# Kernel tuning notes

Hardware: AMD Instinct MI355X
Metric: run time of the kernel (lower is better)

The kernel has to match this reference:

```python
import jax, jax.numpy as jnp
import numpy as np

N = 100000
E = 1600000
IN_C = 256
OUT_C = 64


def setup_inputs() -> dict:
    key = jax.random.key(0)
    k1, k2, k3, k4, k5 = jax.random.split(key, 5)
    x = jax.random.normal(k1, (N, IN_C), dtype=jnp.float32)
    edge_index = jax.random.randint(k2, (2, E), 0, N, dtype=jnp.int64)
    edge_weight = jax.random.uniform(k3, (E,), dtype=jnp.float32)
    # GCNConv linear weight (Glorot-style scale) and bias
    W = jax.random.normal(k4, (IN_C, OUT_C), dtype=jnp.float32) * (1.0 / np.sqrt(IN_C))
    b = jax.random.normal(k5, (OUT_C,), dtype=jnp.float32) * 0.01
    return {"x": x, "edge_index": edge_index, "edge_weight": edge_weight, "W": W, "b": b}


def reference(x, edge_index, edge_weight, W, b):
    n = x.shape[0]
    row, col = edge_index[0], edge_index[1]  # source -> target (PyG source_to_target flow)
    # add self-loops with weight 1.0 (GCNConv default add_self_loops=True)
    loop = jnp.arange(n, dtype=edge_index.dtype)
    row = jnp.concatenate([row, loop])
    col = jnp.concatenate([col, loop])
    ew = jnp.concatenate([edge_weight, jnp.ones((n,), dtype=x.dtype)])
    # symmetric normalization: deg computed on target nodes
    deg = jax.ops.segment_sum(ew, col, num_segments=n)
    dinv = jnp.where(deg > 0, jax.lax.rsqrt(deg), 0.0)
    norm = dinv[row] * ew * dinv[col]  # [E+N]
    # dense linear transform first (fewer FLOPs than transforming per-edge)
    h = x @ W  # [N, OUT_C]
    # gather messages from source, scale, scatter-add to target
    out = jax.ops.segment_sum(norm[:, None] * h[row], col, num_segments=n)
    out = out + b
    # activation is None -> module returns (val, ()); we return val
    return out
```

## Files before the change

### kernel.cpp

```cpp
#include <hip/hip_runtime.h>
#include <hip/hip_fp16.h>


#define BS 256
#define EPB2 2048
#define BSH 8
#define CAP 4608

typedef unsigned long long u64;
typedef unsigned int u32;
typedef unsigned short u16;
typedef unsigned char u8;

typedef __attribute__((ext_vector_type(8))) short bf16x8;
typedef __attribute__((ext_vector_type(4))) float f32x4;

__device__ inline u16 f2bf(float f) {
    u32 u = __float_as_uint(f);
    return (u16)((u + 0x7fffu + ((u >> 16) & 1u)) >> 16);
}
__device__ inline u32 pack2bf(float a, float b) {
    return (u32)f2bf(a) | ((u32)f2bf(b) << 16);
}

#define GBM2 128
#define XAP 40

__global__ __launch_bounds__(BS) void k_g5(const float* __restrict__ x,
                                           const float* __restrict__ W,
                                           u16* __restrict__ hh, int n, int ngemm,
                                           const int* __restrict__ row,
                                           const int* __restrict__ col,
                                           const float* __restrict__ ew,
                                           u32* __restrict__ cursor,
                                           u64* __restrict__ pack,
                                           int nbuck, int e) {
    __shared__ __align__(16) u8 smem[16384];
    const int tid = threadIdx.x;

    if ((int)blockIdx.x >= ngemm) {
        u16* bkt  = (u16*)smem;
        u16* sidx = (u16*)(smem + 4096);
        u32* cnt  = (u32*)(smem + 8192);
        u32* scn  = (u32*)(smem + 10240);
        u32* lpos = (u32*)(smem + 12288);
        u32* gb   = (u32*)(smem + 14336);
        int blk = blockIdx.x - ngemm;
        int base = blk * EPB2;
        int ej = e - base; if (ej > EPB2) ej = EPB2;

        cnt[tid] = 0; cnt[tid + 256] = 0;
        __syncthreads();
#pragma unroll
        for (int j = 0; j < 8; ++j) {
            int lj = j * BS + tid;
            if (lj < ej) {
                int b = col[base + lj] >> BSH;
                bkt[lj] = (u16)b;
                atomicAdd(&cnt[b], 1u);
            }
        }
        __syncthreads();
        scn[tid] = cnt[tid];
        scn[tid + 256] = cnt[tid + 256];
        __syncthreads();
        for (int off = 1; off < 512; off <<= 1) {
            u32 a0 = (tid >= off) ? scn[tid - off] : 0u;
            u32 a1 = scn[tid + 256 - off];
            __syncthreads();
            scn[tid] += a0;
            scn[tid + 256] += a1;
            __syncthreads();
        }
        for (int t = tid; t < 512; t += 256) {
            u32 c = cnt[t];
            lpos[t] = scn[t] - c;
            if (c) gb[t] = atomicAdd(&cursor[t], c);
        }
        __syncthreads();
#pragma unroll
        for (int j = 0; j < 8; ++j) {
            int lj = j * BS + tid;
            if (lj < ej) {
                u32 p = atomicAdd(&lpos[bkt[lj]], 1u);
                sidx[p] = (u16)lj;
            }
        }
        __syncthreads();
        for (int p = tid; p < ej; p += 256) {
            int lj = sidx[p];
            int b = bkt[lj];
            int i = base + lj;
            __half eh = __float2half(ew[i]);
            u64 en = (u64)(u32)row[i]
                   | ((u64)(u32)(col[i] & 255) << 32)
                   | ((u64)(u16)__half_as_ushort(eh) << 48);
            u32 local = (u32)p - (scn[b] - cnt[b]) + gb[b];
            if (local < CAP) pack[(size_t)b * CAP + local] = en;
        }
        return;
    }
    u16* xa = (u16*)smem;
    u16* wt = (u16*)(smem + 10240);
    const int lane = tid & 63;
    const int wid  = tid >> 6;
    const int lr = lane & 15;
    const int lg = lane >> 4;
    const int rb = blockIdx.x * GBM2;
    const int wrow = wid * 32;

    f32x4 acc[2][4];
#pragma unroll
    for (int rt = 0; rt < 2; ++rt)
#pragma unroll
        for (int ct = 0; ct < 4; ++ct) acc[rt][ct] = (f32x4){0.f, 0.f, 0.f, 0.f};

    const int srow = tid >> 1;
    const int skh  = (tid & 1) * 16;
    const int wc   = tid >> 2;
    const int wk   = (tid & 3) * 8;

    for (int kc = 0; kc < 256; kc += 32) {
        {
            int gr = rb + srow; if (gr >= n) gr = n - 1;
            const float4* src = reinterpret_cast<const float4*>(&x[(size_t)gr * 256 + kc + skh]);
            float4 a0 = src[0], a1 = src[1], a2 = src[2], a3 = src[3];
            uint4 v0, v1;
            v0.x = pack2bf(a0.x, a0.y); v0.y = pack2bf(a0.z, a0.w);
            v0.z = pack2bf(a1.x, a1.y); v0.w = pack2bf(a1.z, a1.w);
            v1.x = pack2bf(a2.x, a2.y); v1.y = pack2bf(a2.z, a2.w);
            v1.z = pack2bf(a3.x, a3.y); v1.w = pack2bf(a3.z, a3.w);
            *reinterpret_cast<uint4*>(&xa[srow * XAP + skh]) = v0;
            *reinterpret_cast<uint4*>(&xa[srow * XAP + skh + 8]) = v1;
        }
        {
            float w0 = W[(size_t)(kc + wk + 0) * 64 + wc];
            float w1 = W[(size_t)(kc + wk + 1) * 64 + wc];
            float w2 = W[(size_t)(kc + wk + 2) * 64 + wc];
            float w3 = W[(size_t)(kc + wk + 3) * 64 + wc];
            float w4 = W[(size_t)(kc + wk + 4) * 64 + wc];
            float w5 = W[(size_t)(kc + wk + 5) * 64 + wc];
            float w6 = W[(size_t)(kc + wk + 6) * 64 + wc];
            float w7 = W[(size_t)(kc + wk + 7) * 64 + wc];
            u32* dst = reinterpret_cast<u32*>(&wt[wc * XAP + wk]);
            dst[0] = pack2bf(w0, w1);
            dst[1] = pack2bf(w2, w3);
            dst[2] = pack2bf(w4, w5);
            dst[3] = pack2bf(w6, w7);
        }
        __syncthreads();

        bf16x8 af0 = *reinterpret_cast<const bf16x8*>(&xa[(wrow + lr) * XAP + lg * 8]);
        bf16x8 af1 = *reinterpret_cast<const bf16x8*>(&xa[(wrow + 16 + lr) * XAP + lg * 8]);
#pragma unroll
        for (int ct = 0; ct < 4; ++ct) {
            bf16x8 bfr = *reinterpret_cast<const bf16x8*>(&wt[(ct * 16 + lr) * XAP + lg * 8]);
            acc[0][ct] = __builtin_amdgcn_mfma_f32_16x16x32_bf16(af0, bfr, acc[0][ct], 0, 0, 0);
            acc[1][ct] = __builtin_amdgcn_mfma_f32_16x16x32_bf16(af1, bfr, acc[1][ct], 0, 0, 0);
        }
        __syncthreads();
    }

#pragma unroll
    for (int rt = 0; rt < 2; ++rt) {
        int grow0 = rb + wrow + rt * 16 + lg * 4;
#pragma unroll
        for (int reg = 0; reg < 4; ++reg) {
            int grow = grow0 + reg;
            if (grow < n) {
#pragma unroll
                for (int ct = 0; ct < 4; ++ct) {
                    hh[(size_t)grow * 64 + ct * 16 + lr] =
                        __half_as_ushort(__float2half(acc[rt][ct][reg]));
                }
            }
        }
    }
}

#define MAXB CAP
__global__ __launch_bounds__(512) void k_b2(const u32* __restrict__ cursor,
                                            u64* __restrict__ pack,
                                            float* __restrict__ dinv,
                                            int* __restrict__ offs,
                                            int* __restrict__ ends,
                                            int n, int nbuck) {
    __shared__ u32 lrow[MAXB];
    __shared__ u16 lew[MAXB];
    __shared__ u8  lcl[MAXB];
    __shared__ u32 cnt[256];
    __shared__ float wdeg[256];
    __shared__ u32 pos[256];
    __shared__ float ldsd[256];
    int b = blockIdx.x;
    int tid = threadIdx.x;
    size_t gbase = (size_t)b * CAP;
    int size = (int)cursor[b];
    if (size > MAXB) size = MAXB;
    if (tid < 256) { cnt[tid] = 0; wdeg[tid] = 0.0f; }
    __syncthreads();
    for (int j = tid; j < size; j += 512) {
        u64 en = pack[gbase + j];
        u32 r = (u32)en;
        u32 cl = (u32)(en >> 32) & 255u;
        u16 eh = (u16)(en >> 48);
        lrow[j] = r;
        lcl[j] = (u8)cl;
        lew[j] = eh;
        atomicAdd(&cnt[cl], 1u);
        atomicAdd(&wdeg[cl], __half2float(__ushort_as_half(eh)));
    }
    __syncthreads();
    u32 myc = (tid < 256) ? cnt[tid] : 0;
    for (int off = 1; off < 256; off <<= 1) {
        u32 t = 0;
        if (tid < 256 && tid >= (u32)off) t = cnt[tid - off];
        __syncthreads();
        if (tid < 256) cnt[tid] += t;
        __syncthreads();
    }
    if (tid < 256) {
        u32 st = cnt[tid] - myc;
        pos[tid] = st;
        float dv = rsqrtf(1.0f + wdeg[tid]);
        ldsd[tid] = dv;
        int c = (b << BSH) + tid;
        if (c < n) {
            dinv[c] = dv;
            offs[c] = (int)(gbase + st);
            ends[c] = (int)(gbase + st + myc);
        }
    }
    __syncthreads();
    for (int j = tid; j < size; j += 512) {
        u32 cl = lcl[j];
        u32 r = atomicAdd(&pos[cl], 1u);
        float w = __half2float(__ushort_as_half(lew[j])) * ldsd[cl];
        pack[gbase + r] = ((u64)__float_as_uint(w) << 32) | (u64)lrow[j];
    }
}

__global__ __launch_bounds__(BS) void k_reduce(const u64* __restrict__ sorted,
                                               const int* __restrict__ offs,
                                               const int* __restrict__ ends,
                                               const float* __restrict__ dinv,
                                               const __half2* __restrict__ hh,
                                               const float* __restrict__ bias,
                                               float* __restrict__ out, int n) {
    int node = blockIdx.x * 4 + (threadIdx.x >> 6);
    int lane = threadIdx.x & 63;
    if (node >= n) return;
    int cc  = lane & 31;
    int ehi = lane >> 5;
    int s = offs[node];
    int t = ends[node];
    float ax = 0.0f, ay = 0.0f;
    int j = s;
    for (; j + 7 < t; j += 8) {
        u64 p0 = sorted[j     + ehi];
        u64 p1 = sorted[j + 2 + ehi];
        u64 p2 = sorted[j + 4 + ehi];
        u64 p3 = sorted[j + 6 + ehi];
        int r0 = (int)(u32)p0, r1 = (int)(u32)p1, r2 = (int)(u32)p2, r3 = (int)(u32)p3;
        float n0 = __uint_as_float((u32)(p0 >> 32)) * dinv[r0];
        float n1 = __uint_as_float((u32)(p1 >> 32)) * dinv[r1];
        float n2 = __uint_as_float((u32)(p2 >> 32)) * dinv[r2];
        float n3 = __uint_as_float((u32)(p3 >> 32)) * dinv[r3];
        float2 f0 = __half22float2(hh[(size_t)r0 * 32 + cc]);
        float2 f1 = __half22float2(hh[(size_t)r1 * 32 + cc]);
        float2 f2 = __half22float2(hh[(size_t)r2 * 32 + cc]);
        float2 f3 = __half22float2(hh[(size_t)r3 * 32 + cc]);
        ax += n0 * f0.x; ay += n0 * f0.y;
        ax += n1 * f1.x; ay += n1 * f1.y;
        ax += n2 * f2.x; ay += n2 * f2.y;
        ax += n3 * f3.x; ay += n3 * f3.y;
    }
    for (; j + 1 < t; j += 2) {
        u64 p = sorted[j + ehi];
        int r = (int)(u32)p;
        float nn = __uint_as_float((u32)(p >> 32)) * dinv[r];
        float2 f = __half22float2(hh[(size_t)r * 32 + cc]);
        ax += nn * f.x; ay += nn * f.y;
    }
    if (j < t && ehi == 0) {
        u64 p = sorted[j];
        int r = (int)(u32)p;
        float nn = __uint_as_float((u32)(p >> 32)) * dinv[r];
        float2 f = __half22float2(hh[(size_t)r * 32 + cc]);
        ax += nn * f.x; ay += nn * f.y;
    }
    ax += __shfl_xor(ax, 32);
    ay += __shfl_xor(ay, 32);
    if (ehi == 0) {
        float di = dinv[node];
        float2 fs = __half22float2(hh[(size_t)node * 32 + cc]);
        float2 bb = *reinterpret_cast<const float2*>(&bias[cc * 2]);
        float2 r;
        r.x = ax + di * di * fs.x + bb.x;
        r.y = ay + di * di * fs.y + bb.y;
        reinterpret_cast<float2*>(out)[(size_t)node * 32 + cc] = r;
    }
}

__global__ __launch_bounds__(BS) void k_init_f(float* __restrict__ deg, int n) {
    int i = blockIdx.x * BS + threadIdx.x;
    if (i < n) deg[i] = 1.0f;
}
__global__ __launch_bounds__(BS) void k_count_f(const int* __restrict__ col,
                                                const float* __restrict__ ew,
                                                float* __restrict__ deg, int e) {
    int i = blockIdx.x * BS + threadIdx.x;
    if (i < e) unsafeAtomicAdd(&deg[col[i]], ew[i]);
}
__global__ __launch_bounds__(BS) void k_dinv_f(float* __restrict__ deg, int n) {
    int i = blockIdx.x * BS + threadIdx.x;
    if (i < n) {
        float d = deg[i];
        deg[i] = d > 0.0f ? rsqrtf(d) : 0.0f;
    }
}
__global__ __launch_bounds__(BS) void k_gemm_f(const float* __restrict__ x,
                                               const float* __restrict__ W,
                                               float* __restrict__ h, int n) {
    __shared__ float xsh[4 * 256];
    int b0 = blockIdx.x * 4;
    const float4* xv = reinterpret_cast<const float4*>(x + (size_t)b0 * 256);
    reinterpret_cast<float4*>(xsh)[threadIdx.x] = xv[threadIdx.x];
    __syncthreads();
    int rl = threadIdx.x >> 6;
    int c  = threadIdx.x & 63;
    const float* xr = xsh + rl * 256;
    float acc = 0.0f;
#pragma unroll 8
    for (int k = 0; k < 256; ++k) acc += xr[k] * W[k * 64 + c];
    int r = b0 + rl;
    if (r < n) h[(size_t)r * 64 + c] = acc;
}
__global__ __launch_bounds__(BS) void k_out_init(const float* __restrict__ h,
                                                 const float* __restrict__ dinv,
                                                 const float* __restrict__ bias,
                                                 float* __restrict__ out, int n64) {
    int i = blockIdx.x * BS + threadIdx.x;
    if (i < n64) {
        int r = i >> 6, c = i & 63;
        float di = dinv[r];
        out[i] = bias[c] + di * di * h[i];
    }
}
__global__ __launch_bounds__(BS) void k_scatter(const int* __restrict__ row,
                                                const int* __restrict__ col,
                                                const float* __restrict__ ew,
                                                const float* __restrict__ dinv,
                                                const float* __restrict__ h,
                                                float* __restrict__ out, int e) {
    int idx = blockIdx.x * BS + threadIdx.x;
    int ei = idx >> 6;
    int c  = idx & 63;
    if (ei >= e) return;
    int r = row[ei];
    int t = col[ei];
    float nrm = dinv[r] * ew[ei] * dinv[t];
    unsafeAtomicAdd(&out[(size_t)t * 64 + c], nrm * h[(size_t)r * 64 + c]);
}

extern "C" void kernel_launch(void* const* d_in, const int* in_sizes, int n_in,
                              void* d_out, int out_size, void* d_ws, size_t ws_size,
                              hipStream_t stream) {
    const float* x   = (const float*)d_in[0];
    const int*   ei  = (const int*)d_in[1];
    const float* ew  = (const float*)d_in[2];
    const float* W   = (const float*)d_in[3];
    const float* b   = (const float*)d_in[4];
    float* out = (float*)d_out;

    const int n = in_sizes[0] / 256;
    const int e = in_sizes[1] / 2;
    const int* row = ei;
    const int* col = ei + e;
    const int nbuck = (n + 255) >> 8;
    const int nblk2 = (e + EPB2 - 1) / EPB2;
    const int ngemm = (n + GBM2 - 1) / GBM2;

    size_t off = 0;
    auto alloc = [&](size_t elems) { size_t p = off; off += (elems + 63) & ~63ull; return p; };
    size_t o_cursor = alloc(nbuck);
    size_t o_pack   = alloc((size_t)nbuck * CAP * 2);
    size_t o_offs   = alloc(n);
    size_t o_ends   = alloc(n);
    size_t o_dinv   = alloc(n);
    size_t o_h      = alloc((size_t)n * 32);
    size_t needed = off * 4;

    u32*   wsu = (u32*)d_ws;
    float* wsf = (float*)d_ws;
    int*   wsi = (int*)d_ws;

    if (ws_size >= needed) {
        u32*   cursor = wsu + o_cursor;
        u64*   pack   = (u64*)(wsu + o_pack);
        int*   offs   = wsi + o_offs;
        int*   ends   = wsi + o_ends;
        float* dinv   = wsf + o_dinv;
        u16*   hh     = (u16*)(wsu + o_h);

        hipMemsetAsync(cursor, 0, (size_t)nbuck * 4, stream);
        k_g5<<<ngemm + nblk2, BS, 0, stream>>>(x, W, hh, n, ngemm,
                                               row, col, ew, cursor, pack,
                                               nbuck, e);
        k_b2<<<nbuck, 512, 0, stream>>>(cursor, pack, dinv, offs, ends, n, nbuck);
        k_reduce<<<(n + 3) / 4, BS, 0, stream>>>(pack, offs, ends, dinv,
                                                 (const __half2*)hh, b, out, n);
    } else {
        float* deg = wsf;
        float* h   = wsf + ((n + 63) & ~63);
        const int nb = (n + BS - 1) / BS;
        const int eb = (e + BS - 1) / BS;
        k_init_f<<<nb, BS, 0, stream>>>(deg, n);
        k_count_f<<<eb, BS, 0, stream>>>(col, ew, deg, e);
        k_dinv_f<<<nb, BS, 0, stream>>>(deg, n);
        k_gemm_f<<<(n + 3) / 4, BS, 0, stream>>>(x, W, h, n);
        k_out_init<<<((n * 64) + BS - 1) / BS, BS, 0, stream>>>(h, deg, b, out, n * 64);
        k_scatter<<<((size_t)e * 64 + BS - 1) / BS, BS, 0, stream>>>(row, col, ew, deg, h, out, e);
    }
}
```

Baseline: 134.2 us.

## Stage full W in LDS once and feed x straight from global to MFMA

```diff
diff --git a/kernel.cpp b/kernel.cpp
--- a/kernel.cpp
+++ b/kernel.cpp
@@ -6,6 +6,7 @@
 #define EPB2 2048
 #define BSH 8
 #define CAP 4608
+#define WTS 264
 
 typedef unsigned long long u64;
 typedef unsigned int u32;
@@ -23,10 +24,9 @@
     return (u32)f2bf(a) | ((u32)f2bf(b) << 16);
 }
 
-#define GBM2 128
-#define XAP 40
-
-__global__ __launch_bounds__(BS) void k_g5(const float* __restrict__ x,
+#define GBM3 64
+
+__global__ __launch_bounds__(BS) void k_g6(const float* __restrict__ x,
                                            const float* __restrict__ W,
                                            u16* __restrict__ hh, int n, int ngemm,
                                            const int* __restrict__ row,
@@ -35,7 +35,7 @@
                                            u32* __restrict__ cursor,
                                            u64* __restrict__ pack,
                                            int nbuck, int e) {
-    __shared__ __align__(16) u8 smem[16384];
+    __shared__ __align__(16) u8 smem[33792];
     const int tid = threadIdx.x;
 
     if ((int)blockIdx.x >= ngemm) {
@@ -100,79 +100,58 @@
         }
         return;
     }
-    u16* xa = (u16*)smem;
-    u16* wt = (u16*)(smem + 10240);
+    u16* wt = (u16*)smem;
     const int lane = tid & 63;
     const int wid  = tid >> 6;
     const int lr = lane & 15;
     const int lg = lane >> 4;
-    const int rb = blockIdx.x * GBM2;
-    const int wrow = wid * 32;
-
-    f32x4 acc[2][4];
-#pragma unroll
-    for (int rt = 0; rt < 2; ++rt)
-#pragma unroll
-        for (int ct = 0; ct < 4; ++ct) acc[rt][ct] = (f32x4){0.f, 0.f, 0.f, 0.f};
-
-    const int srow = tid >> 1;
-    const int skh  = (tid & 1) * 16;
-    const int wc   = tid >> 2;
-    const int wk   = (tid & 3) * 8;
-
-    for (int kc = 0; kc < 256; kc += 32) {
-        {
-            int gr = rb + srow; if (gr >= n) gr = n - 1;
-            const float4* src = reinterpret_cast<const float4*>(&x[(size_t)gr * 256 + kc + skh]);
-            float4 a0 = src[0], a1 = src[1], a2 = src[2], a3 = src[3];
-            uint4 v0, v1;
-            v0.x = pack2bf(a0.x, a0.y); v0.y = pack2bf(a0.z, a0.w);
-            v0.z = pack2bf(a1.x, a1.y); v0.w = pack2bf(a1.z, a1.w);
-            v1.x = pack2bf(a2.x, a2.y); v1.y = pack2bf(a2.z, a2.w);
-            v1.z = pack2bf(a3.x, a3.y); v1.w = pack2bf(a3.z, a3.w);
-            *reinterpret_cast<uint4*>(&xa[srow * XAP + skh]) = v0;
-            *reinterpret_cast<uint4*>(&xa[srow * XAP + skh + 8]) = v1;
-        }
-        {
-            float w0 = W[(size_t)(kc + wk + 0) * 64 + wc];
-            float w1 = W[(size_t)(kc + wk + 1) * 64 + wc];
-            float w2 = W[(size_t)(kc + wk + 2) * 64 + wc];
-            float w3 = W[(size_t)(kc + wk + 3) * 64 + wc];
-            float w4 = W[(size_t)(kc + wk + 4) * 64 + wc];
-            float w5 = W[(size_t)(kc + wk + 5) * 64 + wc];
-            float w6 = W[(size_t)(kc + wk + 6) * 64 + wc];
-            float w7 = W[(size_t)(kc + wk + 7) * 64 + wc];
-            u32* dst = reinterpret_cast<u32*>(&wt[wc * XAP + wk]);
-            dst[0] = pack2bf(w0, w1);
-            dst[1] = pack2bf(w2, w3);
-            dst[2] = pack2bf(w4, w5);
-            dst[3] = pack2bf(w6, w7);
-        }
-        __syncthreads();
-
-        bf16x8 af0 = *reinterpret_cast<const bf16x8*>(&xa[(wrow + lr) * XAP + lg * 8]);
-        bf16x8 af1 = *reinterpret_cast<const bf16x8*>(&xa[(wrow + 16 + lr) * XAP + lg * 8]);
+    const int rb = blockIdx.x * GBM3;
+
+#pragma unroll
+    for (int it = 0; it < 32; ++it) {
+        int idx = it * BS + tid;
+        int kp = idx >> 6;
+        int c  = idx & 63;
+        float f0 = W[(size_t)(2 * kp) * 64 + c];
+        float f1 = W[(size_t)(2 * kp + 1) * 64 + c];
+        *reinterpret_cast<u32*>(&wt[c * WTS + 2 * kp]) = pack2bf(f0, f1);
+    }
+    __syncthreads();
+
+    int xrow = rb + wid * 16 + lr;
+    if (xrow >= n) xrow = n - 1;
+    const float* xb = x + (size_t)xrow * 256 + lg * 8;
+
+    f32x4 acc[4];
+#pragma unroll
+    for (int ct = 0; ct < 4; ++ct) acc[ct] = (f32x4){0.f, 0.f, 0.f, 0.f};
+
+#pragma unroll
+    for (int s = 0; s < 8; ++s) {
+        float4 a0 = *reinterpret_cast<const float4*>(xb + s * 32);
+        float4 a1 = *reinterpret_cast<const float4*>(xb + s * 32 + 4);
+        bf16x8 af;
+        u32* afp = reinterpret_cast<u32*>(&af);
+        afp[0] = pack2bf(a0.x, a0.y);
+        afp[1] = pack2bf(a0.z, a0.w);
+        afp[2] = pack2bf(a1.x, a1.y);
+        afp[3] = pack2bf(a1.z, a1.w);
 #pragma unroll
         for (int ct = 0; ct < 4; ++ct) {
-            bf16x8 bfr = *reinterpret_cast<const bf16x8*>(&wt[(ct * 16 + lr) * XAP + lg * 8]);
-            acc[0][ct] = __builtin_amdgcn_mfma_f32_16x16x32_bf16(af0, bfr, acc[0][ct], 0, 0, 0);
-            acc[1][ct] = __builtin_amdgcn_mfma_f32_16x16x32_bf16(af1, bfr, acc[1][ct], 0, 0, 0);
-        }
-        __syncthreads();
-    }
-
-#pragma unroll
-    for (int rt = 0; rt < 2; ++rt) {
-        int grow0 = rb + wrow + rt * 16 + lg * 4;
-#pragma unroll
-        for (int reg = 0; reg < 4; ++reg) {
-            int grow = grow0 + reg;
-            if (grow < n) {
-#pragma unroll
-                for (int ct = 0; ct < 4; ++ct) {
-                    hh[(size_t)grow * 64 + ct * 16 + lr] =
-                        __half_as_ushort(__float2half(acc[rt][ct][reg]));
-                }
+            bf16x8 bfr = *reinterpret_cast<const bf16x8*>(
+                &wt[(ct * 16 + lr) * WTS + s * 32 + lg * 8]);
+            acc[ct] = __builtin_amdgcn_mfma_f32_16x16x32_bf16(af, bfr, acc[ct], 0, 0, 0);
+        }
+    }
+
+#pragma unroll
+    for (int reg = 0; reg < 4; ++reg) {
+        int grow = rb + wid * 16 + lg * 4 + reg;
+        if (grow < n) {
+#pragma unroll
+            for (int ct = 0; ct < 4; ++ct) {
+                hh[(size_t)grow * 64 + ct * 16 + lr] =
+                    __half_as_ushort(__float2half(acc[ct][reg]));
             }
         }
     }
@@ -379,7 +358,7 @@
     const int* col = ei + e;
     const int nbuck = (n + 255) >> 8;
     const int nblk2 = (e + EPB2 - 1) / EPB2;
-    const int ngemm = (n + GBM2 - 1) / GBM2;
+    const int ngemm = (n + GBM3 - 1) / GBM3;
 
     size_t off = 0;
     auto alloc = [&](size_t elems) { size_t p = off; off += (elems + 63) & ~63ull; return p; };
@@ -404,7 +383,7 @@
         u16*   hh     = (u16*)(wsu + o_h);
 
         hipMemsetAsync(cursor, 0, (size_t)nbuck * 4, stream);
-        k_g5<<<ngemm + nblk2, BS, 0, stream>>>(x, W, hh, n, ngemm,
+        k_g6<<<ngemm + nblk2, BS, 0, stream>>>(x, W, hh, n, ngemm,
                                                row, col, ew, cursor, pack,
                                                nbuck, e);
         k_b2<<<nbuck, 512, 0, stream>>>(cursor, pack, dinv, offs, ends, n, nbuck);
```

Result: no change. 134.3 us (+0.1%).

## Split fused GEMM/bucket kernel and widen reduce gathers to 8-byte loads

Applied to the files above, without the earlier changes.

```diff
diff --git a/kernel.cpp b/kernel.cpp
--- a/kernel.cpp
+++ b/kernel.cpp
@@ -26,82 +26,12 @@
 #define GBM2 128
 #define XAP 40
 
-__global__ __launch_bounds__(BS) void k_g5(const float* __restrict__ x,
-                                           const float* __restrict__ W,
-                                           u16* __restrict__ hh, int n, int ngemm,
-                                           const int* __restrict__ row,
-                                           const int* __restrict__ col,
-                                           const float* __restrict__ ew,
-                                           u32* __restrict__ cursor,
-                                           u64* __restrict__ pack,
-                                           int nbuck, int e) {
-    __shared__ __align__(16) u8 smem[16384];
+__global__ __launch_bounds__(BS) void k_gemm_m(const float* __restrict__ x,
+                                               const float* __restrict__ W,
+                                               u16* __restrict__ hh, int n) {
+    __shared__ __align__(16) u16 xa[GBM2 * XAP];
+    __shared__ __align__(16) u16 wt[64 * XAP];
     const int tid = threadIdx.x;
-
-    if ((int)blockIdx.x >= ngemm) {
-        u16* bkt  = (u16*)smem;
-        u16* sidx = (u16*)(smem + 4096);
-        u32* cnt  = (u32*)(smem + 8192);
-        u32* scn  = (u32*)(smem + 10240);
-        u32* lpos = (u32*)(smem + 12288);
-        u32* gb   = (u32*)(smem + 14336);
-        int blk = blockIdx.x - ngemm;
-        int base = blk * EPB2;
-        int ej = e - base; if (ej > EPB2) ej = EPB2;
-
-        cnt[tid] = 0; cnt[tid + 256] = 0;
-        __syncthreads();
-#pragma unroll
-        for (int j = 0; j < 8; ++j) {
-            int lj = j * BS + tid;
-            if (lj < ej) {
-                int b = col[base + lj] >> BSH;
-                bkt[lj] = (u16)b;
-                atomicAdd(&cnt[b], 1u);
-            }
-        }
-        __syncthreads();
-        scn[tid] = cnt[tid];
-        scn[tid + 256] = cnt[tid + 256];
-        __syncthreads();
-        for (int off = 1; off < 512; off <<= 1) {
-            u32 a0 = (tid >= off) ? scn[tid - off] : 0u;
-            u32 a1 = scn[tid + 256 - off];
-            __syncthreads();
-            scn[tid] += a0;
-            scn[tid + 256] += a1;
-            __syncthreads();
-        }
-        for (int t = tid; t < 512; t += 256) {
-            u32 c = cnt[t];
-            lpos[t] = scn[t] - c;
-            if (c) gb[t] = atomicAdd(&cursor[t], c);
-        }
-        __syncthreads();
-#pragma unroll
-        for (int j = 0; j < 8; ++j) {
-            int lj = j * BS + tid;
-            if (lj < ej) {
-                u32 p = atomicAdd(&lpos[bkt[lj]], 1u);
-                sidx[p] = (u16)lj;
-            }
-        }
-        __syncthreads();
-        for (int p = tid; p < ej; p += 256) {
-            int lj = sidx[p];
-            int b = bkt[lj];
-            int i = base + lj;
-            __half eh = __float2half(ew[i]);
-            u64 en = (u64)(u32)row[i]
-                   | ((u64)(u32)(col[i] & 255) << 32)
-                   | ((u64)(u16)__half_as_ushort(eh) << 48);
-            u32 local = (u32)p - (scn[b] - cnt[b]) + gb[b];
-            if (local < CAP) pack[(size_t)b * CAP + local] = en;
-        }
-        return;
-    }
-    u16* xa = (u16*)smem;
-    u16* wt = (u16*)(smem + 10240);
     const int lane = tid & 63;
     const int wid  = tid >> 6;
     const int lr = lane & 15;
@@ -175,6 +105,73 @@
                 }
             }
         }
+    }
+}
+
+__global__ __launch_bounds__(BS) void k_scat(const int* __restrict__ row,
+                                             const int* __restrict__ col,
+                                             const float* __restrict__ ew,
+                                             u32* __restrict__ cursor,
+                                             u64* __restrict__ pack,
+                                             int nbuck, int e) {
+    __shared__ u16 bkt[2048];
+    __shared__ u16 sidx[2048];
+    __shared__ u32 cnt[512];
+    __shared__ u32 scn[512];
+    __shared__ u32 lpos[512];
+    __shared__ u32 gb[512];
+    const int tid = threadIdx.x;
+    int base = blockIdx.x * EPB2;
+    int ej = e - base; if (ej > EPB2) ej = EPB2;
+
+    cnt[tid] = 0; cnt[tid + 256] = 0;
+    __syncthreads();
+#pragma unroll
+    for (int j = 0; j < 8; ++j) {
+        int lj = j * BS + tid;
+        if (lj < ej) {
+            int b = col[base + lj] >> BSH;
+            bkt[lj] = (u16)b;
+            atomicAdd(&cnt[b], 1u);
+        }
+    }
+    __syncthreads();
+    scn[tid] = cnt[tid];
+    scn[tid + 256] = cnt[tid + 256];
+    __syncthreads();
+    for (int off = 1; off < 512; off <<= 1) {
+        u32 a0 = (tid >= off) ? scn[tid - off] : 0u;
+        u32 a1 = scn[tid + 256 - off];
+        __syncthreads();
+        scn[tid] += a0;
+        scn[tid + 256] += a1;
+        __syncthreads();
+    }
+    for (int t = tid; t < 512; t += 256) {
+        u32 c = cnt[t];
+        lpos[t] = scn[t] - c;
+        if (c) gb[t] = atomicAdd(&cursor[t], c);
+    }
+    __syncthreads();
+#pragma unroll
+    for (int j = 0; j < 8; ++j) {
+        int lj = j * BS + tid;
+        if (lj < ej) {
+            u32 p = atomicAdd(&lpos[bkt[lj]], 1u);
+            sidx[p] = (u16)lj;
+        }
+    }
+    __syncthreads();
+    for (int p = tid; p < ej; p += 256) {
+        int lj = sidx[p];
+        int b = bkt[lj];
+        int i = base + lj;
+        __half eh = __float2half(ew[i]);
+        u64 en = (u64)(u32)row[i]
+               | ((u64)(u32)(col[i] & 255) << 32)
+               | ((u64)(u16)__half_as_ushort(eh) << 48);
+        u32 local = (u32)p - (scn[b] - cnt[b]) + gb[b];
+        if (local < CAP) pack[(size_t)b * CAP + local] = en;
     }
 }
 
@@ -244,61 +241,69 @@
                                                const int* __restrict__ offs,
                                                const int* __restrict__ ends,
                                                const float* __restrict__ dinv,
-                                               const __half2* __restrict__ hh,
+                                               const uint2* __restrict__ hq,
                                                const float* __restrict__ bias,
                                                float* __restrict__ out, int n) {
     int node = blockIdx.x * 4 + (threadIdx.x >> 6);
     int lane = threadIdx.x & 63;
     if (node >= n) return;
-    int cc  = lane & 31;
-    int ehi = lane >> 5;
+    int q   = lane & 15;
+    int ehi = lane >> 4;
     int s = offs[node];
     int t = ends[node];
-    float ax = 0.0f, ay = 0.0f;
+    float a0 = 0.f, a1 = 0.f, a2 = 0.f, a3 = 0.f;
     int j = s;
     for (; j + 7 < t; j += 8) {
-        u64 p0 = sorted[j     + ehi];
-        u64 p1 = sorted[j + 2 + ehi];
-        u64 p2 = sorted[j + 4 + ehi];
-        u64 p3 = sorted[j + 6 + ehi];
-        int r0 = (int)(u32)p0, r1 = (int)(u32)p1, r2 = (int)(u32)p2, r3 = (int)(u32)p3;
-        float n0 = __uint_as_float((u32)(p0 >> 32)) * dinv[r0];
-        float n1 = __uint_as_float((u32)(p1 >> 32)) * dinv[r1];
-        float n2 = __uint_as_float((u32)(p2 >> 32)) * dinv[r2];
-        float n3 = __uint_as_float((u32)(p3 >> 32)) * dinv[r3];
-        float2 f0 = __half22float2(hh[(size_t)r0 * 32 + cc]);
-        float2 f1 = __half22float2(hh[(size_t)r1 * 32 + cc]);
-        float2 f2 = __half22float2(hh[(size_t)r2 * 32 + cc]);
-        float2 f3 = __half22float2(hh[(size_t)r3 * 32 + cc]);
-        ax += n0 * f0.x; ay += n0 * f0.y;
-        ax += n1 * f1.x; ay += n1 * f1.y;
-        ax += n2 * f2.x; ay += n2 * f2.y;
-        ax += n3 * f3.x; ay += n3 * f3.y;
-    }
-    for (; j + 1 < t; j += 2) {
+        u64 pA = sorted[j + ehi];
+        u64 pB = sorted[j + 4 + ehi];
+        int rA = (int)(u32)pA, rB = (int)(u32)pB;
+        uint2 vA = hq[(size_t)rA * 16 + q];
+        uint2 vB = hq[(size_t)rB * 16 + q];
+        float nA = __uint_as_float((u32)(pA >> 32)) * dinv[rA];
+        float nB = __uint_as_float((u32)(pB >> 32)) * dinv[rB];
+        float2 fA0 = __half22float2(*reinterpret_cast<__half2*>(&vA.x));
+        float2 fA1 = __half22float2(*reinterpret_cast<__half2*>(&vA.y));
+        float2 fB0 = __half22float2(*reinterpret_cast<__half2*>(&vB.x));
+        float2 fB1 = __half22float2(*reinterpret_cast<__half2*>(&vB.y));
+        a0 += nA * fA0.x; a1 += nA * fA0.y; a2 += nA * fA1.x; a3 += nA * fA1.y;
+        a0 += nB * fB0.x; a1 += nB * fB0.y; a2 += nB * fB1.x; a3 += nB * fB1.y;
+    }
+    for (; j + 3 < t; j += 4) {
         u64 p = sorted[j + ehi];
         int r = (int)(u32)p;
+        uint2 v = hq[(size_t)r * 16 + q];
         float nn = __uint_as_float((u32)(p >> 32)) * dinv[r];
-        float2 f = __half22float2(hh[(size_t)r * 32 + cc]);
-        ax += nn * f.x; ay += nn * f.y;
-    }
-    if (j < t && ehi == 0) {
-        u64 p = sorted[j];
-        int r = (int)(u32)p;
-        float nn = __uint_as_float((u32)(p >> 32)) * dinv[r];
-        float2 f = __half22float2(hh[(size_t)r * 32 + cc]);
-        ax += nn * f.x; ay += nn * f.y;
-    }
-    ax += __shfl_xor(ax, 32);
-    ay += __shfl_xor(ay, 32);
+        float2 f0 = __half22float2(*reinterpret_cast<__half2*>(&v.x));
+        float2 f1 = __half22float2(*reinterpret_cast<__half2*>(&v.y));
+        a0 += nn * f0.x; a1 += nn * f0.y; a2 += nn * f1.x; a3 += nn * f1.y;
+    }
+    for (; j < t; ++j) {
+        if (ehi == 0) {
+            u64 p = sorted[j];
+            int r = (int)(u32)p;
+            uint2 v = hq[(size_t)r * 16 + q];
+            float nn = __uint_as_float((u32)(p >> 32)) * dinv[r];
+            float2 f0 = __half22float2(*reinterpret_cast<__half2*>(&v.x));
+            float2 f1 = __half22float2(*reinterpret_cast<__half2*>(&v.y));
+            a0 += nn * f0.x; a1 += nn * f0.y; a2 += nn * f1.x; a3 += nn * f1.y;
+        }
+    }
+    a0 += __shfl_xor(a0, 16); a1 += __shfl_xor(a1, 16);
+    a2 += __shfl_xor(a2, 16); a3 += __shfl_xor(a3, 16);
+    a0 += __shfl_xor(a0, 32); a1 += __shfl_xor(a1, 32);
+    a2 += __shfl_xor(a2, 32); a3 += __shfl_xor(a3, 32);
     if (ehi == 0) {
         float di = dinv[node];
-        float2 fs = __half22float2(hh[(size_t)node * 32 + cc]);
-        float2 bb = *reinterpret_cast<const float2*>(&bias[cc * 2]);
-        float2 r;
-        r.x = ax + di * di * fs.x + bb.x;
-        r.y = ay + di * di * fs.y + bb.y;
-        reinterpret_cast<float2*>(out)[(size_t)node * 32 + cc] = r;
+        uint2 vs = hq[(size_t)node * 16 + q];
+        float2 s0 = __half22float2(*reinterpret_cast<__half2*>(&vs.x));
+        float2 s1 = __half22float2(*reinterpret_cast<__half2*>(&vs.y));
+        float4 bb = *reinterpret_cast<const float4*>(&bias[q * 4]);
+        float4 o;
+        o.x = a0 + di * di * s0.x + bb.x;
+        o.y = a1 + di * di * s0.y + bb.y;
+        o.z = a2 + di * di * s1.x + bb.z;
+        o.w = a3 + di * di * s1.y + bb.w;
+        *reinterpret_cast<float4*>(&out[(size_t)node * 64 + q * 4]) = o;
     }
 }
 
@@ -404,12 +409,11 @@
         u16*   hh     = (u16*)(wsu + o_h);
 
         hipMemsetAsync(cursor, 0, (size_t)nbuck * 4, stream);
-        k_g5<<<ngemm + nblk2, BS, 0, stream>>>(x, W, hh, n, ngemm,
-                                               row, col, ew, cursor, pack,
-                                               nbuck, e);
+        k_gemm_m<<<ngemm, BS, 0, stream>>>(x, W, hh, n);
+        k_scat<<<nblk2, BS, 0, stream>>>(row, col, ew, cursor, pack, nbuck, e);
         k_b2<<<nbuck, 512, 0, stream>>>(cursor, pack, dinv, offs, ends, n, nbuck);
         k_reduce<<<(n + 3) / 4, BS, 0, stream>>>(pack, offs, ends, dinv,
-                                                 (const __half2*)hh, b, out, n);
+                                                 (const uint2*)hh, b, out, n);
     } else {
         float* deg = wsf;
         float* h   = wsf + ((n + 63) & ~63);
```

Result: slower. 152.3 us (+13.5%).
